# Performance work log

Hardware: AMD Instinct MI355X
Metric: run time of the kernel (lower is better)

## Reference

```python
import jax, jax.numpy as jnp
import numpy as np

N_NODES = 2048
UNITS = 64
IN_DIM = 64
K_DIFF = 2  # max_diffusion_step


def _rw_norm_t(adj):
    # random-walk normalize D^{-1}(A+I), then transpose (as in forward())
    a = adj + jnp.eye(adj.shape[0], dtype=adj.dtype)
    d = jnp.sum(a, axis=1)
    d_inv = jnp.where(d > 0, 1.0 / jnp.where(d > 0, d, 1.0), 0.0)
    return (d_inv[:, None] * a).T


def _gconv(x_cat, adj_t, W, b):
    # x_cat: (B, N, F). Chebyshev-like diffusion: x0, A x0, 2 A x1 - x0, ...
    x0 = x_cat
    xs = [x0]
    x1 = jnp.einsum('nm,bmf->bnf', adj_t, x0)
    xs.append(x1)
    for _ in range(2, K_DIFF + 1):
        x2 = 2.0 * jnp.einsum('nm,bmf->bnf', adj_t, x1) - x0
        xs.append(x2)
        x0, x1 = x1, x2
    x = jnp.stack(xs, axis=-1)  # (B, N, F, K+1) -> matches torch permute(3,1,2,0)
    B, N, F, K = x.shape
    x = x.reshape(B * N, F * K)
    out = x @ W + b
    return out.reshape(B, N, -1)


def setup_inputs() -> dict:
    key = jax.random.key(0)
    ks = jax.random.split(key, 6)
    B = 64
    inputs = jax.random.normal(ks[0], (B, N_NODES * IN_DIM), dtype=jnp.float32)
    hx = jax.random.normal(ks[1], (B, N_NODES * UNITS), dtype=jnp.float32)
    adj = jax.random.uniform(ks[2], (N_NODES, N_NODES), dtype=jnp.float32)
    in_sz = IN_DIM + UNITS
    nm = K_DIFF + 1
    scale = float(np.sqrt(2.0 / (in_sz * nm + 2 * UNITS)))  # xavier-ish
    W_ru = jax.random.normal(ks[3], (in_sz * nm, 2 * UNITS), dtype=jnp.float32) * scale
    b_ru = jnp.ones((2 * UNITS,), dtype=jnp.float32)  # bias_start=1.0
    W_c = jax.random.normal(ks[4], (in_sz * nm, UNITS), dtype=jnp.float32) * scale
    b_c = jnp.zeros((UNITS,), dtype=jnp.float32)
    return {"inputs": inputs, "hx": hx, "adj": adj,
            "W_ru": W_ru, "b_ru": b_ru, "W_c": W_c, "b_c": b_c}


def reference(inputs, hx, adj, W_ru, b_ru, W_c, b_c):
    B = inputs.shape[0]
    x = inputs.reshape(B, N_NODES, IN_DIM)
    h = hx.reshape(B, N_NODES, UNITS)
    adj_t = _rw_norm_t(adj)
    # r/u gates via graph conv + sigmoid
    ru = jax.nn.sigmoid(_gconv(jnp.concatenate([x, h], axis=-1), adj_t, W_ru, b_ru))
    r, u = ru[..., :UNITS], ru[..., UNITS:]
    # candidate state
    c = jnp.tanh(_gconv(jnp.concatenate([x, r * h], axis=-1), adj_t, W_c, b_c))
    new_state = u * h + (1.0 - u) * c
    return new_state.reshape(B, N_NODES * UNITS)
```

## Files before the change

### kernel.cpp

```cpp
#include <hip/hip_runtime.h>
#include <math.h>

typedef __attribute__((ext_vector_type(8))) short short8;
typedef __attribute__((ext_vector_type(4))) float float4v;
typedef __attribute__((ext_vector_type(4))) unsigned short ushort4v;
typedef unsigned short u16;
typedef unsigned int u32;

#define NB 64
#define NN 2048
#define FD 128
#define UD 64
#define KT 384

__device__ __forceinline__ u16 f2bf(float f) {
    unsigned int u = __float_as_uint(f);
    u += 0x7fffu + ((u >> 16) & 1u);
    return (u16)(u >> 16);
}
__device__ __forceinline__ float bf2f(u16 s) {
    return __uint_as_float(((unsigned int)s) << 16);
}
__device__ __forceinline__ float sigmoidf_(float x) {
    return 1.0f / (1.0f + expf(-x));
}
__device__ __forceinline__ void gl2lds16(const u16* g, u16* l) {
    __builtin_amdgcn_global_load_lds((const __attribute__((address_space(1))) unsigned int*)g,
                                     (__attribute__((address_space(3))) unsigned int*)l,
                                     16, 0, 0);
}

__global__ void k_rownorm(const float* __restrict__ adj, float* __restrict__ d_inv) {
    int m = blockIdx.x;
    const float4v* row = (const float4v*)(adj + (size_t)m * NN);
    float s = 0.f;
    for (int i = threadIdx.x; i < NN / 4; i += 256) {
        float4v v = row[i];
        s += v.x + v.y + v.z + v.w;
    }
    __shared__ float red[4];
    for (int off = 32; off; off >>= 1) s += __shfl_down(s, off, 64);
    if ((threadIdx.x & 63) == 0) red[threadIdx.x >> 6] = s;
    __syncthreads();
    if (threadIdx.x == 0) {
        float t = red[0] + red[1] + red[2] + red[3] + 1.0f;
        d_inv[m] = 1.0f / t;
    }
}

__global__ void k_adjT(const float* __restrict__ adj, const float* __restrict__ d_inv,
                       u16* __restrict__ adjT) {
    __shared__ u16 T[64 * 72];
    int m0 = blockIdx.x * 64;
    int n0 = blockIdx.y * 64;
    int t = threadIdx.x;
    for (int p = 0; p < 4; ++p) {
        int idx = t + 256 * p;
        int i  = idx >> 4;
        int n4 = idx & 15;
        int m = m0 + i;
        float4v v = *(const float4v*)(adj + (size_t)m * NN + n0 + n4 * 4);
        float di = d_inv[m];
        float vv[4] = {v.x, v.y, v.z, v.w};
#pragma unroll
        for (int j = 0; j < 4; ++j) {
            int n = n0 + n4 * 4 + j;
            float a = vv[j] + ((m == n) ? 1.0f : 0.0f);
            T[(n4 * 4 + j) * 72 + i] = f2bf(a * di);
        }
    }
    __syncthreads();
    for (int p = 0; p < 2; ++p) {
        int idx = t + 256 * p;
        int n  = idx >> 3;
        int m8 = (idx & 7) * 8;
        *(short8*)(adjT + (size_t)(n0 + n) * NN + m0 + m8) = *(const short8*)(T + n * 72 + m8);
    }
}

__global__ void k_reorderW(const float* __restrict__ W, u16* __restrict__ Wt, int OD) {
    int idx = blockIdx.x * 256 + threadIdx.x;
    if (idx >= KT * OD) return;
    int o  = idx % OD;
    int kp = idx / OD;
    int kd = kp >> 7, f = kp & 127;
    Wt[(size_t)o * KT + kp] = f2bf(W[(size_t)(f * 3 + kd) * OD + o]);
}

__global__ void k_xcat(const float* __restrict__ x, const float* __restrict__ h,
                       u16* __restrict__ X0c) {
    __shared__ u16 T[128 * 136];
    int m0 = blockIdx.x * 128;
    int b  = blockIdx.y;
    int t = threadIdx.x;
    const float* srcs[2] = { x + (size_t)b * (NN * 64), h + (size_t)b * (NN * 64) };
    for (int s = 0; s < 2; ++s) {
        const float* src = srcs[s];
        for (int p = 0; p < 8; ++p) {
            int idx = t + 256 * p;
            int mi = idx >> 4;
            int f4 = idx & 15;
            float4v v = *(const float4v*)(src + (size_t)(m0 + mi) * 64 + f4 * 4);
            float vv[4] = {v.x, v.y, v.z, v.w};
#pragma unroll
            for (int j = 0; j < 4; ++j)
                T[(s * 64 + f4 * 4 + j) * 136 + mi] = f2bf(vv[j]);
        }
    }
    __syncthreads();
    for (int p = 0; p < 8; ++p) {
        int idx = t + 256 * p;
        int f  = idx >> 4;
        int m8 = (idx & 15) * 8;
        *(short8*)(X0c + ((size_t)(b * FD + f)) * NN + m0 + m8) = *(const short8*)(T + f * 136 + m8);
    }
}

__global__ __launch_bounds__(256)
void k_gemm_big(const u16* __restrict__ A, const u16* __restrict__ Bc,
                u16* __restrict__ Cc, const u16* __restrict__ Sub, int mode, int cBlocks) {
    __shared__ u16 SM[128 * 130];
    u16* A0 = SM;          u16* A1 = SM + 4096;
    u16* B0 = SM + 8192;   u16* B1 = SM + 12288;

    int id = blockIdx.x + cBlocks * blockIdx.y;
    int band = cBlocks >> 3;
    int g = id & 7;
    int s = id >> 3;
    int cb = g * band + (s % band);
    int nb = s / band;
    int c0 = cb * 128;
    int n0 = nb * 128;

    int t = threadIdx.x;
    int wave = t >> 6, lane = t & 63;
    int wr = (wave >> 1) * 64, wc = (wave & 1) * 64;
    int lr = lane & 15, q = lane >> 4;

    int r0 = t >> 2;
    int cc = (t & 3) * 8;
    const u16* ga0 = A  + (size_t)(n0 + r0) * 2048 + cc;
    const u16* ga1 = A  + (size_t)(n0 + r0 + 64) * 2048 + cc;
    const u16* gb0 = Bc + (size_t)(c0 + r0) * 2048 + cc;
    const u16* gb1 = Bc + (size_t)(c0 + r0 + 64) * 2048 + cc;

    float4v acc[4][4];
#pragma unroll
    for (int i = 0; i < 4; ++i)
#pragma unroll
        for (int j = 0; j < 4; ++j) { acc[i][j].x = 0.f; acc[i][j].y = 0.f; acc[i][j].z = 0.f; acc[i][j].w = 0.f; }

    gl2lds16(ga0, A0 + t * 8); gl2lds16(ga1, A0 + (t + 256) * 8);
    gl2lds16(gb0, B0 + t * 8); gl2lds16(gb1, B0 + (t + 256) * 8);

#pragma unroll 2
    for (int it = 0; it < 64; ++it) {
        u16* Ac = (it & 1) ? A1 : A0;
        u16* Bs = (it & 1) ? B1 : B0;
        __syncthreads();
        if (it + 1 < 64) {
            int ko = (it + 1) * 32;
            u16* An = (it & 1) ? A0 : A1;
            u16* Bn = (it & 1) ? B0 : B1;
            gl2lds16(ga0 + ko, An + t * 8); gl2lds16(ga1 + ko, An + (t + 256) * 8);
            gl2lds16(gb0 + ko, Bn + t * 8); gl2lds16(gb1 + ko, Bn + (t + 256) * 8);
        }
        short8 af[4], bfr[4];
#pragma unroll
        for (int i = 0; i < 4; ++i) af[i]  = *(const short8*)(Ac + (wr + 16 * i + lr) * 32 + q * 8);
#pragma unroll
        for (int j = 0; j < 4; ++j) bfr[j] = *(const short8*)(Bs + (wc + 16 * j + lr) * 32 + q * 8);
#pragma unroll
        for (int i = 0; i < 4; ++i)
#pragma unroll
            for (int j = 0; j < 4; ++j)
                acc[i][j] = __builtin_amdgcn_mfma_f32_16x16x32_bf16(af[i], bfr[j], acc[i][j], 0, 0, 0);
    }

    __syncthreads();
#pragma unroll
    for (int i = 0; i < 4; ++i) {
        int nl = wr + 16 * i + q * 4;
#pragma unroll
        for (int j = 0; j < 4; ++j) {
            int cl = wc + 16 * j + lr;
            float4v v = acc[i][j];
            ushort4v pk;
#pragma unroll
            for (int r = 0; r < 4; ++r) pk[r] = f2bf(v[r]);
            *(ushort4v*)(SM + cl * 130 + nl) = pk;
        }
    }
    __syncthreads();
#pragma unroll
    for (int p = 0; p < 2; ++p) {
        int idx = t + 256 * p;
        int cl = idx >> 2;
        int nc = (idx & 3) * 8;
        u16* dst = Cc + (size_t)(c0 + cl) * 2048 + n0 + nc;
        const u16* sub = Sub + (size_t)(c0 + cl) * 2048 + n0 + nc;
        const u16* srcl = SM + cl * 130 + nc;
#pragma unroll
        for (int u = 0; u < 4; ++u) {
            short8 v = *(const short8*)(srcl + u * 32);
            if (mode == 1) {
                short8 sv = *(const short8*)(sub + u * 32);
                short8 o;
#pragma unroll
                for (int e = 0; e < 8; ++e)
                    o[e] = (short)f2bf(2.f * bf2f((u16)v[e]) - bf2f((u16)sv[e]));
                *(short8*)(dst + u * 32) = o;
            } else {
                *(short8*)(dst + u * 32) = v;
            }
        }
    }
}

__global__ __launch_bounds__(256)
void k_ruW(const u16* __restrict__ X0c, const u16* __restrict__ X1c, const u16* __restrict__ X2c,
           const u16* __restrict__ Wt, const float* __restrict__ bias,
           const float* __restrict__ hx,
           u16* __restrict__ RH0c, float* __restrict__ Utc) {
    __shared__ u16 As[128 * 40];
    __shared__ u16 Bs[128 * 32];
    int rt = blockIdx.x;
    int b  = rt >> 4;
    int m0 = (rt & 15) * 128;
    int t = threadIdx.x;
    int wave = t >> 6, lane = t & 63;
    int wr = (wave >> 1) * 64, wc = (wave & 1) * 64;
    int lr = lane & 15, q = lane >> 4;
    const u16* Xs[3] = {X0c, X1c, X2c};
    int f2 = t & 15;
    int m8 = (t >> 4) * 8;
    const u16* gw = Wt + (size_t)(t >> 2) * KT + (t & 3) * 8;
    u16* lw0 = Bs + t * 8;  u16* lw1 = Bs + (t + 256) * 8;
    const u16* gw1 = Wt + (size_t)((t >> 2) + 64) * KT + (t & 3) * 8;

    float4v acc[4][4];
#pragma unroll
    for (int i = 0; i < 4; ++i)
#pragma unroll
        for (int j = 0; j < 4; ++j) { acc[i][j].x = 0.f; acc[i][j].y = 0.f; acc[i][j].z = 0.f; acc[i][j].w = 0.f; }

    for (int it = 0; it < 12; ++it) {
        int k0 = it * 32;
        int kd = k0 >> 7, fb = k0 & 127;
        const u16* src = Xs[kd] + ((size_t)(b * FD + fb)) * NN + m0;
        gl2lds16(gw  + k0, lw0);
        gl2lds16(gw1 + k0, lw1);
        short8 v0 = *(const short8*)(src + (size_t)(2 * f2)     * NN + m8);
        short8 v1 = *(const short8*)(src + (size_t)(2 * f2 + 1) * NN + m8);
#pragma unroll
        for (int e = 0; e < 8; ++e)
            *(u32*)(As + (m8 + e) * 40 + 2 * f2) = (u32)(u16)v0[e] | ((u32)(u16)v1[e] << 16);
        __syncthreads();
        short8 af[4], bfr[4];
#pragma unroll
        for (int i = 0; i < 4; ++i) af[i]  = *(const short8*)(As + (wr + 16 * i + lr) * 40 + q * 8);
#pragma unroll
        for (int j = 0; j < 4; ++j) bfr[j] = *(const short8*)(Bs + (wc + 16 * j + lr) * 32 + q * 8);
#pragma unroll
        for (int i = 0; i < 4; ++i)
#pragma unroll
            for (int j = 0; j < 4; ++j)
                acc[i][j] = __builtin_amdgcn_mfma_f32_16x16x32_bf16(af[i], bfr[j], acc[i][j], 0, 0, 0);
        __syncthreads();
    }
#pragma unroll
    for (int i = 0; i < 4; ++i) {
        int m = m0 + wr + 16 * i + q * 4;
#pragma unroll
        for (int j = 0; j < 4; ++j) {
            int o = wc + 16 * j + lr;
            float bia = bias[o];
            float4v v = acc[i][j];
            if (o < 64) {
                ushort4v pk;
#pragma unroll
                for (int r = 0; r < 4; ++r) {
                    float s = sigmoidf_(v[r] + bia);
                    float hh = hx[(size_t)b * (NN * 64) + (size_t)(m + r) * 64 + o];
                    pk[r] = f2bf(s * hh);
                }
                *(ushort4v*)(RH0c + ((size_t)(b * UD + o)) * NN + m) = pk;
            } else {
                int g = o - 64;
                float4v u;
#pragma unroll
                for (int r = 0; r < 4; ++r) u[r] = sigmoidf_(v[r] + bia);
                *(float4v*)(Utc + ((size_t)(b * UD + g)) * NN + m) = u;
            }
        }
    }
}

__global__ __launch_bounds__(256)
void k_cW(const u16* __restrict__ X0c, const u16* __restrict__ X1c, const u16* __restrict__ X2c,
          const u16* __restrict__ RH0c, const u16* __restrict__ RH1c, const u16* __restrict__ RH2c,
          const u16* __restrict__ Wt, const float* __restrict__ bias,
          const float* __restrict__ hx, const float* __restrict__ Utc,
          float* __restrict__ out) {
    __shared__ u16 As[256 * 40];
    __shared__ u16 Bs[64 * 32];
    int rt = blockIdx.x;
    int b  = rt >> 3;
    int m0 = (rt & 7) * 256;
    int t = threadIdx.x;
    int wave = t >> 6, lane = t & 63;
    int lr = lane & 15, q = lane >> 4;
    const u16* Xs[3] = {X0c, X1c, X2c};
    const u16* Rs[3] = {RH0c, RH1c, RH2c};
    const u16* gw = Wt + (size_t)(t >> 2) * KT + (t & 3) * 8;
    u16* lw = Bs + t * 8;

    float4v acc[4][4];
#pragma unroll
    for (int i = 0; i < 4; ++i)
#pragma unroll
        for (int j = 0; j < 4; ++j) { acc[i][j].x = 0.f; acc[i][j].y = 0.f; acc[i][j].z = 0.f; acc[i][j].w = 0.f; }

    for (int it = 0; it < 12; ++it) {
        int k0 = it * 32;
        int kd = k0 >> 7, fb = k0 & 127;
        const u16* src;
        if (fb < 64) src = Xs[kd] + ((size_t)(b * FD + fb)) * NN + m0;
        else         src = Rs[kd] + ((size_t)(b * UD + (fb - 64))) * NN + m0;
        gl2lds16(gw + k0, lw);
#pragma unroll
        for (int p = 0; p < 2; ++p) {
            int idx = t + 256 * p;
            int f2 = idx & 15;
            int m8 = (idx >> 4) * 8;
            short8 v0 = *(const short8*)(src + (size_t)(2 * f2)     * NN + m8);
            short8 v1 = *(const short8*)(src + (size_t)(2 * f2 + 1) * NN + m8);
#pragma unroll
            for (int e = 0; e < 8; ++e)
                *(u32*)(As + (m8 + e) * 40 + 2 * f2) = (u32)(u16)v0[e] | ((u32)(u16)v1[e] << 16);
        }
        __syncthreads();
        short8 af[4], bfr[4];
#pragma unroll
        for (int i = 0; i < 4; ++i) af[i]  = *(const short8*)(As + (64 * wave + 16 * i + lr) * 40 + q * 8);
#pragma unroll
        for (int j = 0; j < 4; ++j) bfr[j] = *(const short8*)(Bs + (16 * j + lr) * 32 + q * 8);
#pragma unroll
        for (int i = 0; i < 4; ++i)
#pragma unroll
            for (int j = 0; j < 4; ++j)
                acc[i][j] = __builtin_amdgcn_mfma_f32_16x16x32_bf16(af[i], bfr[j], acc[i][j], 0, 0, 0);
        __syncthreads();
    }
#pragma unroll
    for (int i = 0; i < 4; ++i) {
        int m = m0 + 64 * wave + 16 * i + q * 4;
#pragma unroll
        for (int j = 0; j < 4; ++j) {
            int o = 16 * j + lr;
            float bia = bias[o];
            float4v v = acc[i][j];
            float4v u = *(const float4v*)(Utc + ((size_t)(b * UD + o)) * NN + m);
#pragma unroll
            for (int r = 0; r < 4; ++r) {
                float c = tanhf(v[r] + bia);
                size_t idx = (size_t)b * (NN * 64) + (size_t)(m + r) * 64 + o;
                float hh = hx[idx];
                out[idx] = u[r] * hh + (1.0f - u[r]) * c;
            }
        }
    }
}

extern "C" void kernel_launch(void* const* d_in, const int* in_sizes, int n_in,
                              void* d_out, int out_size, void* d_ws, size_t ws_size,
                              hipStream_t stream) {
    const float* x    = (const float*)d_in[0];
    const float* hx   = (const float*)d_in[1];
    const float* adj  = (const float*)d_in[2];
    const float* W_ru = (const float*)d_in[3];
    const float* b_ru = (const float*)d_in[4];
    const float* W_c  = (const float*)d_in[5];
    const float* b_c  = (const float*)d_in[6];
    float* out = (float*)d_out;

    char* ws = (char*)d_ws;
    size_t off = 0;
    auto alloc = [&](size_t bytes) -> void* {
        void* p = ws + off;
        off += (bytes + 255) & ~(size_t)255;
        return p;
    };
    float* d_inv = (float*)alloc((size_t)NN * 4);
    u16* adjT  = (u16*)alloc((size_t)NN * NN * 2);
    u16* Wt_ru = (u16*)alloc((size_t)FD * KT * 2);
    u16* Wt_c  = (u16*)alloc((size_t)UD * KT * 2);
    u16* X0c = (u16*)alloc((size_t)NB * FD * NN * 2);
    u16* X1c = (u16*)alloc((size_t)NB * FD * NN * 2);
    u16* X2c = (u16*)alloc((size_t)NB * FD * NN * 2);
    u16* RH0c = (u16*)alloc((size_t)NB * UD * NN * 2);
    u16* RH1c = (u16*)alloc((size_t)NB * UD * NN * 2);
    u16* RH2c = (u16*)alloc((size_t)NB * UD * NN * 2);
    float* Utc = (float*)alloc((size_t)NB * UD * NN * 4);

    k_rownorm<<<dim3(NN), dim3(256), 0, stream>>>(adj, d_inv);
    k_adjT<<<dim3(32, 32), dim3(256), 0, stream>>>(adj, d_inv, adjT);
    k_reorderW<<<dim3((KT * FD + 255) / 256), dim3(256), 0, stream>>>(W_ru, Wt_ru, FD);
    k_reorderW<<<dim3((KT * UD + 255) / 256), dim3(256), 0, stream>>>(W_c, Wt_c, UD);
    k_xcat<<<dim3(16, NB), dim3(256), 0, stream>>>(x, hx, X0c);
    k_gemm_big<<<dim3(64, 16), dim3(256), 0, stream>>>(adjT, X0c, X1c, X0c, 0, 64);
    k_gemm_big<<<dim3(64, 16), dim3(256), 0, stream>>>(adjT, X1c, X2c, X0c, 1, 64);
    k_ruW<<<dim3(1024), dim3(256), 0, stream>>>(X0c, X1c, X2c, Wt_ru, b_ru, hx, RH0c, Utc);
    k_gemm_big<<<dim3(32, 16), dim3(256), 0, stream>>>(adjT, RH0c, RH1c, RH0c, 0, 32);
    k_gemm_big<<<dim3(32, 16), dim3(256), 0, stream>>>(adjT, RH1c, RH2c, RH0c, 1, 32);
    k_cW<<<dim3(512), dim3(256), 0, stream>>>(X0c, X1c, X2c, RH0c, RH1c, RH2c, Wt_c, b_c, hx, Utc, out);
}
```

Measured before the change: 520.1 us.

## Enlarge diffusion GEMM tile to 128x256 using 32x32x16 MFMA

```diff
diff --git a/kernel.cpp b/kernel.cpp
--- a/kernel.cpp
+++ b/kernel.cpp
@@ -3,6 +3,7 @@
 
 typedef __attribute__((ext_vector_type(8))) short short8;
 typedef __attribute__((ext_vector_type(4))) float float4v;
+typedef __attribute__((ext_vector_type(16))) float float16v;
 typedef __attribute__((ext_vector_type(4))) unsigned short ushort4v;
 typedef unsigned short u16;
 typedef unsigned int u32;
@@ -116,12 +117,12 @@
     }
 }
 
-__global__ __launch_bounds__(256)
+__global__ __launch_bounds__(256, 2)
 void k_gemm_big(const u16* __restrict__ A, const u16* __restrict__ Bc,
                 u16* __restrict__ Cc, const u16* __restrict__ Sub, int mode, int cBlocks) {
-    __shared__ u16 SM[128 * 130];
-    u16* A0 = SM;          u16* A1 = SM + 4096;
-    u16* B0 = SM + 8192;   u16* B1 = SM + 12288;
+    __shared__ u16 SM[24576];
+    u16* A0 = SM;           u16* A1 = SM + 4096;
+    u16* B0 = SM + 8192;    u16* B1 = SM + 16384;
 
     int id = blockIdx.x + cBlocks * blockIdx.y;
     int band = cBlocks >> 3;
@@ -129,29 +130,33 @@
     int s = id >> 3;
     int cb = g * band + (s % band);
     int nb = s / band;
-    int c0 = cb * 128;
+    int c0 = cb * 256;
     int n0 = nb * 128;
 
     int t = threadIdx.x;
     int wave = t >> 6, lane = t & 63;
-    int wr = (wave >> 1) * 64, wc = (wave & 1) * 64;
-    int lr = lane & 15, q = lane >> 4;
+    int wy = wave & 1;
+    int wx = wave >> 1;
+    int ln = lane & 31, hi = lane >> 5;
 
     int r0 = t >> 2;
-    int cc = (t & 3) * 8;
-    const u16* ga0 = A  + (size_t)(n0 + r0) * 2048 + cc;
-    const u16* ga1 = A  + (size_t)(n0 + r0 + 64) * 2048 + cc;
-    const u16* gb0 = Bc + (size_t)(c0 + r0) * 2048 + cc;
-    const u16* gb1 = Bc + (size_t)(c0 + r0 + 64) * 2048 + cc;
-
-    float4v acc[4][4];
+    int kc = (t & 3) * 8;
+    const u16* ga = A  + (size_t)(n0 + r0) * 2048 + kc;
+    const u16* gb = Bc + (size_t)(c0 + r0) * 2048 + kc;
+
+    float16v acc[4][2];
 #pragma unroll
     for (int i = 0; i < 4; ++i)
 #pragma unroll
-        for (int j = 0; j < 4; ++j) { acc[i][j].x = 0.f; acc[i][j].y = 0.f; acc[i][j].z = 0.f; acc[i][j].w = 0.f; }
-
-    gl2lds16(ga0, A0 + t * 8); gl2lds16(ga1, A0 + (t + 256) * 8);
-    gl2lds16(gb0, B0 + t * 8); gl2lds16(gb1, B0 + (t + 256) * 8);
+        for (int j = 0; j < 2; ++j)
+#pragma unroll
+            for (int e = 0; e < 16; ++e) acc[i][j][e] = 0.f;
+
+    gl2lds16(ga, A0 + t * 8);
+    gl2lds16(ga + (size_t)64 * 2048, A0 + (t + 256) * 8);
+#pragma unroll
+    for (int i = 0; i < 4; ++i)
+        gl2lds16(gb + (size_t)(64 * i) * 2048, B0 + (t + 256 * i) * 8);
 
 #pragma unroll 2
     for (int it = 0; it < 64; ++it) {
@@ -162,56 +167,64 @@
             int ko = (it + 1) * 32;
             u16* An = (it & 1) ? A0 : A1;
             u16* Bn = (it & 1) ? B0 : B1;
-            gl2lds16(ga0 + ko, An + t * 8); gl2lds16(ga1 + ko, An + (t + 256) * 8);
-            gl2lds16(gb0 + ko, Bn + t * 8); gl2lds16(gb1 + ko, Bn + (t + 256) * 8);
-        }
-        short8 af[4], bfr[4];
-#pragma unroll
-        for (int i = 0; i < 4; ++i) af[i]  = *(const short8*)(Ac + (wr + 16 * i + lr) * 32 + q * 8);
-#pragma unroll
-        for (int j = 0; j < 4; ++j) bfr[j] = *(const short8*)(Bs + (wc + 16 * j + lr) * 32 + q * 8);
-#pragma unroll
-        for (int i = 0; i < 4; ++i)
-#pragma unroll
-            for (int j = 0; j < 4; ++j)
-                acc[i][j] = __builtin_amdgcn_mfma_f32_16x16x32_bf16(af[i], bfr[j], acc[i][j], 0, 0, 0);
+            gl2lds16(ga + ko, An + t * 8);
+            gl2lds16(ga + (size_t)64 * 2048 + ko, An + (t + 256) * 8);
+#pragma unroll
+            for (int i = 0; i < 4; ++i)
+                gl2lds16(gb + (size_t)(64 * i) * 2048 + ko, Bn + (t + 256 * i) * 8);
+        }
+        short8 fa[2][4], fb[2][2];
+#pragma unroll
+        for (int ks = 0; ks < 2; ++ks) {
+#pragma unroll
+            for (int mt = 0; mt < 4; ++mt)
+                fa[ks][mt] = *(const short8*)(Bs + (wx * 128 + mt * 32 + ln) * 32 + ks * 16 + hi * 8);
+#pragma unroll
+            for (int nt = 0; nt < 2; ++nt)
+                fb[ks][nt] = *(const short8*)(Ac + (wy * 64 + nt * 32 + ln) * 32 + ks * 16 + hi * 8);
+        }
+#pragma unroll
+        for (int ks = 0; ks < 2; ++ks)
+#pragma unroll
+            for (int mt = 0; mt < 4; ++mt)
+#pragma unroll
+                for (int nt = 0; nt < 2; ++nt)
+                    acc[mt][nt] = __builtin_amdgcn_mfma_f32_32x32x16_bf16(fa[ks][mt], fb[ks][nt], acc[mt][nt], 0, 0, 0);
     }
 
     __syncthreads();
 #pragma unroll
-    for (int i = 0; i < 4; ++i) {
-        int nl = wr + 16 * i + q * 4;
-#pragma unroll
-        for (int j = 0; j < 4; ++j) {
-            int cl = wc + 16 * j + lr;
-            float4v v = acc[i][j];
-            ushort4v pk;
-#pragma unroll
-            for (int r = 0; r < 4; ++r) pk[r] = f2bf(v[r]);
-            *(ushort4v*)(SM + cl * 130 + nl) = pk;
-        }
-    }
-    __syncthreads();
-#pragma unroll
     for (int p = 0; p < 2; ++p) {
-        int idx = t + 256 * p;
-        int cl = idx >> 2;
-        int nc = (idx & 3) * 8;
-        u16* dst = Cc + (size_t)(c0 + cl) * 2048 + n0 + nc;
-        const u16* sub = Sub + (size_t)(c0 + cl) * 2048 + n0 + nc;
-        const u16* srcl = SM + cl * 130 + nc;
-#pragma unroll
-        for (int u = 0; u < 4; ++u) {
-            short8 v = *(const short8*)(srcl + u * 32);
+        if (p) __syncthreads();
+        if (wx == p) {
+#pragma unroll
+            for (int mt = 0; mt < 4; ++mt)
+#pragma unroll
+                for (int nt = 0; nt < 2; ++nt)
+#pragma unroll
+                    for (int e = 0; e < 16; ++e) {
+                        int cl = mt * 32 + 4 * hi + 8 * (e >> 2) + (e & 3);
+                        int nl = wy * 64 + nt * 32 + ln;
+                        SM[cl * 136 + nl] = f2bf(acc[mt][nt][e]);
+                    }
+        }
+        __syncthreads();
+        int r = t >> 1, half = t & 1;
+        const u16* srow = SM + r * 136 + half * 64;
+        u16* drow = Cc + (size_t)(c0 + p * 128 + r) * 2048 + n0 + half * 64;
+        const u16* subr = Sub + (size_t)(c0 + p * 128 + r) * 2048 + n0 + half * 64;
+#pragma unroll
+        for (int u = 0; u < 8; ++u) {
+            short8 v = *(const short8*)(srow + u * 8);
             if (mode == 1) {
-                short8 sv = *(const short8*)(sub + u * 32);
+                short8 sv = *(const short8*)(subr + u * 8);
                 short8 o;
 #pragma unroll
                 for (int e = 0; e < 8; ++e)
                     o[e] = (short)f2bf(2.f * bf2f((u16)v[e]) - bf2f((u16)sv[e]));
-                *(short8*)(dst + u * 32) = o;
+                *(short8*)(drow + u * 8) = o;
             } else {
-                *(short8*)(dst + u * 32) = v;
+                *(short8*)(drow + u * 8) = v;
             }
         }
     }
@@ -286,11 +299,11 @@
                 }
                 *(ushort4v*)(RH0c + ((size_t)(b * UD + o)) * NN + m) = pk;
             } else {
-                int g = o - 64;
+                int gg = o - 64;
                 float4v u;
 #pragma unroll
                 for (int r = 0; r < 4; ++r) u[r] = sigmoidf_(v[r] + bia);
-                *(float4v*)(Utc + ((size_t)(b * UD + g)) * NN + m) = u;
+                *(float4v*)(Utc + ((size_t)(b * UD + gg)) * NN + m) = u;
             }
         }
     }
@@ -408,10 +421,10 @@
     k_reorderW<<<dim3((KT * FD + 255) / 256), dim3(256), 0, stream>>>(W_ru, Wt_ru, FD);
     k_reorderW<<<dim3((KT * UD + 255) / 256), dim3(256), 0, stream>>>(W_c, Wt_c, UD);
     k_xcat<<<dim3(16, NB), dim3(256), 0, stream>>>(x, hx, X0c);
-    k_gemm_big<<<dim3(64, 16), dim3(256), 0, stream>>>(adjT, X0c, X1c, X0c, 0, 64);
-    k_gemm_big<<<dim3(64, 16), dim3(256), 0, stream>>>(adjT, X1c, X2c, X0c, 1, 64);
+    k_gemm_big<<<dim3(32, 16), dim3(256), 0, stream>>>(adjT, X0c, X1c, X0c, 0, 32);
+    k_gemm_big<<<dim3(32, 16), dim3(256), 0, stream>>>(adjT, X1c, X2c, X0c, 1, 32);
     k_ruW<<<dim3(1024), dim3(256), 0, stream>>>(X0c, X1c, X2c, Wt_ru, b_ru, hx, RH0c, Utc);
-    k_gemm_big<<<dim3(32, 16), dim3(256), 0, stream>>>(adjT, RH0c, RH1c, RH0c, 0, 32);
-    k_gemm_big<<<dim3(32, 16), dim3(256), 0, stream>>>(adjT, RH1c, RH2c, RH0c, 1, 32);
+    k_gemm_big<<<dim3(16, 16), dim3(256), 0, stream>>>(adjT, RH0c, RH1c, RH0c, 0, 16);
+    k_gemm_big<<<dim3(16, 16), dim3(256), 0, stream>>>(adjT, RH1c, RH2c, RH0c, 1, 16);
     k_cW<<<dim3(512), dim3(256), 0, stream>>>(X0c, X1c, X2c, RH0c, RH1c, RH2c, Wt_c, b_c, hx, Utc, out);
 }
```

Measured after the change: 533.9 us. 2.6% more time.
